# Performance work log

Measured on AMD Instinct MI355X. Metric: run time of the kernel, lower is better.

Reference implementation:

```python
import jax, jax.numpy as jnp
import numpy as np

N_NODES = 25000
N_EDGES = 400000
MUL0 = 16      # multiplicity of 0e
MUL1 = 8       # multiplicity of 1o
H = 64         # radial MLP width (= dist_embedding dim)
WEIGHT_NUMEL = MUL0*MUL0 + MUL0*MUL1 + MUL1*MUL1 + MUL1*MUL0  # 576
NUM_NEIGHBORS = 16
INV_SQRT3 = 0.57735026918962576  # w3j normalization for l=1 paths
PW0 = (1.0/24.0)**0.5  # path weight, 0e out: alpha = dim(0e)/ (16+8)
PW1 = (3.0/24.0)**0.5  # path weight, 1o out: alpha = dim(1o)/ (16+8)
SILU_NORM = 1.6791767923989418  # e3nn normalize2mom factor for silu


def _radial_mlp(d, W1, W2):
    # e3nn FullyConnectedNet([H, H, WEIGHT_NUMEL], silu): x @ W / sqrt(fan_in),
    # activation normalized to unit second moment.
    h = SILU_NORM * jax.nn.silu(d @ W1 / jnp.sqrt(jnp.asarray(H, d.dtype)))
    return h @ W2 / jnp.sqrt(jnp.asarray(H, d.dtype))


def _tensor_product(x, y, w):
    # x: [E, 40] gathered node feats; y: [E, 4] edge_attr; w: [E, 576]
    x0 = x[:, :MUL0]                        # [E,16]  0e
    x1 = x[:, MUL0:].reshape(-1, MUL1, 3)   # [E,8,3] 1o
    y0 = y[:, :1]                           # [E,1]   0e
    y1 = y[:, 1:4]                          # [E,3]   1o
    s = MUL0*MUL0
    w1 = w[:, :s].reshape(-1, MUL0, MUL0)                       # 0e*0e->0e
    w2 = w[:, s:s+MUL0*MUL1].reshape(-1, MUL0, MUL1)            # 0e*1o->1o
    s2 = s + MUL0*MUL1
    w3 = w[:, s2:s2+MUL1*MUL1].reshape(-1, MUL1, MUL1)          # 1o*0e->1o
    s3 = s2 + MUL1*MUL1
    w4 = w[:, s3:].reshape(-1, MUL1, MUL0)                      # 1o*1o->0e
    out0 = PW0 * (jnp.einsum('eu,euw->ew', x0 * y0, w1)
                  + INV_SQRT3 * jnp.einsum('eui,ei,euw->ew', x1, y1, w4))
    out1 = PW1 * INV_SQRT3 * (jnp.einsum('eu,ej,euw->ewj', x0, y1, w2)
                              + jnp.einsum('eui,euw->ewi', x1 * y0[:, :, None], w3))
    return jnp.concatenate([out0, out1.reshape(-1, MUL1*3)], axis=1)  # [E,40]


def setup_inputs() -> dict:
    key = jax.random.key(0)
    ks = jax.random.split(key, 7)
    node_input = jax.random.normal(ks[0], (N_NODES, MUL0 + 3*MUL1), jnp.float32)
    edge_src = jax.random.randint(ks[1], (N_EDGES,), 0, N_NODES)
    edge_dst = jax.random.randint(ks[2], (N_EDGES,), 0, N_NODES)
    edge_attr = jax.random.normal(ks[3], (N_EDGES, 4), jnp.float32)
    dist_embedding = jax.random.normal(ks[4], (N_EDGES, H), jnp.float32)
    W1 = jax.random.normal(ks[5], (H, H), jnp.float32)
    W2 = jax.random.normal(ks[6], (H, WEIGHT_NUMEL), jnp.float32)
    return {"node_input": node_input, "edge_src": edge_src, "edge_dst": edge_dst,
            "edge_attr": edge_attr, "dist_embedding": dist_embedding,
            "W1": W1, "W2": W2}


def reference(node_input, edge_src, edge_dst, edge_attr, dist_embedding, W1, W2):
    tp_weights = _radial_mlp(dist_embedding, W1, W2)            # [E,576]
    edge_features = _tensor_product(node_input[edge_dst], edge_attr, tp_weights)
    node_features = jax.ops.segment_sum(edge_features, edge_src,
                                        num_segments=N_NODES)
    return node_features / jnp.sqrt(jnp.asarray(NUM_NEIGHBORS, node_features.dtype))
```

## Files before the change

kernel.cpp:

```cpp
#include <hip/hip_runtime.h>

#define N_NODES 25000
#define N_EDGES 400000

static constexpr float INV_SQRT3 = 0.5773502691896257f;
static constexpr float PW0 = 0.20412414523193154f;
static constexpr float PW1 = 0.35355339059327373f;
static constexpr float SILU_NORM = 1.6791767923989418f;
static constexpr float SCC = 0.03125f;
static constexpr float KP1C = PW1 * INV_SQRT3 * SCC;
static constexpr float Q4C  = PW0 * INV_SQRT3 * SCC;

typedef __attribute__((ext_vector_type(8))) short bf16x8;
typedef __attribute__((ext_vector_type(4))) float f32x4;

__device__ __forceinline__ unsigned short f2bf(float x) {
    unsigned int u = __float_as_uint(x);
    u += 0x7FFFu + ((u >> 16) & 1u);
    return (unsigned short)(u >> 16);
}

__device__ __forceinline__ bf16x8 pack8(const float* p) {
    float4 a = *(const float4*)p, b = *(const float4*)(p + 4);
    bf16x8 r;
    r[0] = (short)f2bf(a.x); r[1] = (short)f2bf(a.y);
    r[2] = (short)f2bf(a.z); r[3] = (short)f2bf(a.w);
    r[4] = (short)f2bf(b.x); r[5] = (short)f2bf(b.y);
    r[6] = (short)f2bf(b.z); r[7] = (short)f2bf(b.w);
    return r;
}

#define WS_CNT  0
#define WS_CUR  25000
#define WS_EIDX 50000
#define WS_W1T  450000
#define WS_W2T  452048
#define WS_REQ_BYTES ((size_t)(452048 + 18432) * 4)

__global__ __launch_bounds__(256) void k_prep(const float* __restrict__ W1,
                                              const float* __restrict__ W2,
                                              unsigned short* __restrict__ W1Tg,
                                              unsigned short* __restrict__ W2Tg)
{
    const int id = blockIdx.x * 256 + threadIdx.x;
    if (id < 64 * 64) {
        const int n = id >> 6, j = id & 63;
        W1Tg[n * 64 + (j ^ ((n & 7) << 3))] = f2bf(W1[j * 64 + n]);
    }
    if (id < 576 * 64) {
        const int n = id / 64, k = id % 64;
        W2Tg[n * 64 + (k ^ ((n & 7) << 3))] = f2bf(W2[k * 576 + n]);
    }
}

__global__ __launch_bounds__(256) void k_hist(const int* __restrict__ edge_src,
                                              int* __restrict__ cnt)
{
    const int e = blockIdx.x * 256 + threadIdx.x;
    if (e < N_EDGES) atomicAdd(&cnt[edge_src[e]], 1);
}

__global__ __launch_bounds__(1024) void k_scan(const int* __restrict__ cnt,
                                               int* __restrict__ cur)
{
    __shared__ int sa[1024], sb[1024];
    const int t = threadIdx.x;
    const int base = t * 25;
    int loc[25];
    int s = 0;
#pragma unroll
    for (int q = 0; q < 25; ++q) {
        const int idx = base + q;
        const int v = (idx < N_NODES) ? cnt[idx] : 0;
        loc[q] = s; s += v;
    }
    sa[t] = s;
    __syncthreads();
    int* sp = sa; int* dp = sb;
    for (int d = 1; d < 1024; d <<= 1) {
        int v = sp[t];
        if (t >= d) v += sp[t - d];
        dp[t] = v;
        __syncthreads();
        int* tmp = sp; sp = dp; dp = tmp;
    }
    const int excl = sp[t] - s;
#pragma unroll
    for (int q = 0; q < 25; ++q) {
        const int idx = base + q;
        if (idx < N_NODES) cur[idx] = excl + loc[q];
    }
}

__global__ __launch_bounds__(256) void k_scatter(const int* __restrict__ edge_src,
                                                 int* __restrict__ cur,
                                                 int* __restrict__ eidx)
{
    const int e = blockIdx.x * 256 + threadIdx.x;
    if (e < N_EDGES) {
        const int pos = atomicAdd(&cur[edge_src[e]], 1);
        eidx[pos] = e;
    }
}

__global__ __launch_bounds__(256) void k_conv(
    const float* __restrict__ node_input,
    const int* __restrict__ edge_src,
    const int* __restrict__ edge_dst,
    const float* __restrict__ edge_attr,
    const float* __restrict__ dist_embedding,
    const unsigned short* __restrict__ W1Tg,
    const unsigned short* __restrict__ W2Tg,
    const int* __restrict__ eidx_g,
    float* __restrict__ out)
{
    __shared__ __align__(16) unsigned short sB[288 * 64];
    __shared__ __align__(16) unsigned short sH[64 * 64];
    __shared__ float xq_s[64 * 56];
    __shared__ float racc[64 * 40];
    __shared__ int   eidx_s[64], src_s[64], p0_s[64];

    const int t  = threadIdx.x;
    const int pb = blockIdx.x * 64;
    const int w = t >> 6, lane = t & 63;
    const int kgrp = lane >> 4;
    const int cl = lane & 15;

    if (t < 64) {
        const int eid = eidx_g[pb + t];
        eidx_s[t] = eid;
        src_s[t]  = edge_src[eid];
        const int dst = edge_dst[eid];
        const float4* xr = (const float4*)(node_input + (size_t)dst * 40);
        float* xd = xq_s + t * 56;
        float xx[40];
#pragma unroll
        for (int i = 0; i < 10; ++i) {
            float4 v = xr[i];
            xx[i*4+0] = v.x; xx[i*4+1] = v.y; xx[i*4+2] = v.z; xx[i*4+3] = v.w;
            *(float4*)(xd + i * 4) = v;
        }
        const float4 yv = *(const float4*)(edge_attr + (size_t)eid * 4);
        xd[48] = PW0 * SCC * yv.x;
        xd[49] = KP1C * yv.x;
        xd[50] = yv.y; xd[51] = yv.z; xd[52] = yv.w;
#pragma unroll
        for (int u = 0; u < 8; ++u)
            xd[40 + u] = yv.y * xx[16 + u*3] + yv.z * xx[16 + u*3 + 1] + yv.w * xx[16 + u*3 + 2];
    }
    {
        const uint4* s = (const uint4*)W1Tg;
        uint4* d = (uint4*)sB;
        d[t] = s[t];
        d[t + 256] = s[t + 256];
    }
    for (int i = t; i < 64 * 40; i += 256) racc[i] = 0.f;
    __syncthreads();

    {
        const int er = w * 16 + cl;
        const float* dp = dist_embedding + (size_t)eidx_s[er] * 64 + kgrp * 8;
        bf16x8 a0 = pack8(dp);
        bf16x8 a1 = pack8(dp + 32);
        const int bx = (cl & 7) << 3;
#pragma unroll
        for (int nt = 0; nt < 4; ++nt) {
            const int n = nt * 16 + cl;
            const unsigned short* bp = sB + n * 64;
            bf16x8 b0 = *(const bf16x8*)(bp + ((kgrp * 8) ^ bx));
            bf16x8 b1 = *(const bf16x8*)(bp + ((32 + kgrp * 8) ^ bx));
            f32x4 c = {0.f, 0.f, 0.f, 0.f};
            c = __builtin_amdgcn_mfma_f32_16x16x32_bf16(a0, b0, c, 0, 0, 0);
            c = __builtin_amdgcn_mfma_f32_16x16x32_bf16(a1, b1, c, 0, 0, 0);
#pragma unroll
            for (int r = 0; r < 4; ++r) {
                const float zz = 0.125f * c[r];
                const float h = SILU_NORM * __fdividef(zz, 1.f + __expf(-zz));
                const int hr = w * 16 + kgrp * 4 + r;
                const int hc = nt * 16 + cl;
                sH[hr * 64 + (hc ^ ((hr & 7) << 3))] = f2bf(h);
            }
        }
    }
    if (t < 64) {
        int p = t;
        while (p > 0 && src_s[p - 1] == src_s[t]) --p;
        p0_s[t] = p;
    }
    __syncthreads();

    const int arow = w * 16 + cl;
    const unsigned short* ap = sH + arow * 64;
    const int ax = (cl & 7) << 3;
    bf16x8 A0 = *(const bf16x8*)(ap + ((kgrp * 8) ^ ax));
    bf16x8 A1 = *(const bf16x8*)(ap + ((32 + kgrp * 8) ^ ax));

    float r1a[4] = {0,0,0,0}, r4a[4] = {0,0,0,0}, Tt[4] = {0,0,0,0};
    float P0[4] = {0,0,0,0}, P1[4] = {0,0,0,0}, P2[4] = {0,0,0,0};
    const int e0 = w * 16 + kgrp * 4;

#pragma unroll
    for (int ph = 0; ph < 2; ++ph) {
        {
            const uint4* gs = (const uint4*)(W2Tg + (size_t)ph * 18432);
            uint4* ds = (uint4*)sB;
#pragma unroll
            for (int i = 0; i < 9; ++i) ds[t + i * 256] = gs[t + i * 256];
        }
        __syncthreads();
        const int bx = (cl & 7) << 3;
#pragma unroll
        for (int nt = 0; nt < 18; ++nt) {
            const int bcol = nt * 16 + cl;
            const unsigned short* bp = sB + bcol * 64;
            bf16x8 B0 = *(const bf16x8*)(bp + ((kgrp * 8) ^ bx));
            bf16x8 B1 = *(const bf16x8*)(bp + ((32 + kgrp * 8) ^ bx));
            f32x4 c = {0.f, 0.f, 0.f, 0.f};
            c = __builtin_amdgcn_mfma_f32_16x16x32_bf16(A0, B0, c, 0, 0, 0);
            c = __builtin_amdgcn_mfma_f32_16x16x32_bf16(A1, B1, c, 0, 0, 0);
            const int gnt = ph * 18 + nt;
            if (gnt < 16) {
#pragma unroll
                for (int r = 0; r < 4; ++r) r1a[r] += xq_s[(e0 + r) * 56 + gnt] * c[r];
            } else if (gnt < 24) {
                const int u = (gnt - 16) * 2 + ((lane >> 3) & 1);
#pragma unroll
                for (int r = 0; r < 4; ++r) Tt[r] += xq_s[(e0 + r) * 56 + u] * c[r];
            } else if (gnt < 28) {
                const int u = (gnt - 24) * 2 + ((lane >> 3) & 1);
#pragma unroll
                for (int r = 0; r < 4; ++r) {
                    const float* xp = xq_s + (e0 + r) * 56 + 16 + u * 3;
                    P0[r] += xp[0] * c[r];
                    P1[r] += xp[1] * c[r];
                    P2[r] += xp[2] * c[r];
                }
            } else {
                const int u = gnt - 28;
#pragma unroll
                for (int r = 0; r < 4; ++r) r4a[r] += xq_s[(e0 + r) * 56 + 40 + u] * c[r];
            }
        }
        __syncthreads();
    }

#pragma unroll
    for (int r = 0; r < 4; ++r) {
        const int e = e0 + r;
        const float v = xq_s[e * 56 + 48] * r1a[r] + Q4C * r4a[r];
        atomicAdd(&racc[p0_s[e] * 40 + cl], v);
    }
#pragma unroll
    for (int r = 0; r < 4; ++r) {
        Tt[r] += __shfl_xor(Tt[r], 8);
        P0[r] += __shfl_xor(P0[r], 8);
        P1[r] += __shfl_xor(P1[r], 8);
        P2[r] += __shfl_xor(P2[r], 8);
    }
    if ((lane & 8) == 0) {
        const int wo = lane & 7;
#pragma unroll
        for (int r = 0; r < 4; ++r) {
            const int e = e0 + r;
            const float q3  = xq_s[e * 56 + 49];
            const float y1x = xq_s[e * 56 + 50];
            const float y1y = xq_s[e * 56 + 51];
            const float y1z = xq_s[e * 56 + 52];
            float* rp = &racc[p0_s[e] * 40 + 16 + wo * 3];
            atomicAdd(rp + 0, KP1C * y1x * Tt[r] + q3 * P0[r]);
            atomicAdd(rp + 1, KP1C * y1y * Tt[r] + q3 * P1[r]);
            atomicAdd(rp + 2, KP1C * y1z * Tt[r] + q3 * P2[r]);
        }
    }
    __syncthreads();
    if (t < 64 && p0_s[t] == t) {
        float* op = out + (size_t)src_s[t] * 40;
        const float* rp = racc + t * 40;
#pragma unroll
        for (int cc = 0; cc < 40; ++cc) atomicAdd(op + cc, rp[cc]);
    }
}

template <int NC>
__device__ __forceinline__ void gemm_cols(const float* __restrict__ base,
                                          const float (&h)[64], float (&w)[NC]) {
#pragma unroll
    for (int i = 0; i < NC; ++i) w[i] = 0.f;
#pragma unroll
    for (int k = 0; k < 64; ++k) {
        const float4* r4 = (const float4*)(base + k * 576);
        const float hk = h[k];
#pragma unroll
        for (int q = 0; q < NC / 4; ++q) {
            float4 a = r4[q];
            w[q * 4 + 0] += hk * a.x;  w[q * 4 + 1] += hk * a.y;
            w[q * 4 + 2] += hk * a.z;  w[q * 4 + 3] += hk * a.w;
        }
    }
}

__global__ __launch_bounds__(256) void conv_atomic(
    const float* __restrict__ node_input,
    const int* __restrict__ edge_src,
    const int* __restrict__ edge_dst,
    const float* __restrict__ edge_attr,
    const float* __restrict__ dist_embedding,
    const float* __restrict__ W1,
    const float* __restrict__ W2,
    float* __restrict__ out)
{
    __shared__ float sX[256 * 44];
    const int e = blockIdx.x * 256 + threadIdx.x;
    if (e >= N_EDGES) return;
    float* xs = &sX[threadIdx.x * 44];

    float z[64];
#pragma unroll
    for (int k = 0; k < 64; ++k) z[k] = 0.f;
    const float4* dp = (const float4*)(dist_embedding + (size_t)e * 64);
#pragma unroll 2
    for (int j4 = 0; j4 < 16; ++j4) {
        float4 d4 = dp[j4];
        float dj[4] = {d4.x, d4.y, d4.z, d4.w};
#pragma unroll
        for (int r = 0; r < 4; ++r) {
            const float4* w1r = (const float4*)(W1 + (j4 * 4 + r) * 64);
            const float dv = dj[r];
#pragma unroll
            for (int k4 = 0; k4 < 16; ++k4) {
                float4 a = w1r[k4];
                z[k4 * 4 + 0] += dv * a.x; z[k4 * 4 + 1] += dv * a.y;
                z[k4 * 4 + 2] += dv * a.z; z[k4 * 4 + 3] += dv * a.w;
            }
        }
    }
    float h[64];
#pragma unroll
    for (int k = 0; k < 64; ++k) {
        const float zz = 0.125f * z[k];
        h[k] = SILU_NORM * __fdividef(zz, 1.f + __expf(-zz));
    }
    const int dst = edge_dst[e];
    const float4* xr = (const float4*)(node_input + (size_t)dst * 40);
    float4* xd = (float4*)xs;
#pragma unroll
    for (int i = 0; i < 10; ++i) xd[i] = xr[i];
    const float4 yv = *(const float4*)(edge_attr + (size_t)e * 4);
    const float q0 = PW0 * yv.x * SCC;
    const float q4 = PW0 * INV_SQRT3 * SCC;
    const float q20 = KP1C * yv.y, q21 = KP1C * yv.z, q22 = KP1C * yv.w;
    const float q3 = KP1C * yv.x;
    float o0[16], o1[24];
#pragma unroll
    for (int i = 0; i < 16; ++i) o0[i] = 0.f;
#pragma unroll
    for (int i = 0; i < 24; ++i) o1[i] = 0.f;
#pragma unroll 1
    for (int u = 0; u < 16; ++u) {
        float w[16];
        gemm_cols<16>(W2 + u * 16, h, w);
        const float coef = q0 * xs[u];
#pragma unroll
        for (int i = 0; i < 16; ++i) o0[i] += coef * w[i];
    }
#pragma unroll 1
    for (int u = 0; u < 16; ++u) {
        float w[8];
        gemm_cols<8>(W2 + 256 + u * 8, h, w);
        const float xv = xs[u];
        const float c0 = q20 * xv, c1 = q21 * xv, c2 = q22 * xv;
#pragma unroll
        for (int i = 0; i < 8; ++i) {
            o1[i * 3 + 0] += c0 * w[i]; o1[i * 3 + 1] += c1 * w[i]; o1[i * 3 + 2] += c2 * w[i];
        }
    }
#pragma unroll 1
    for (int u = 0; u < 8; ++u) {
        float w[8];
        gemm_cols<8>(W2 + 384 + u * 8, h, w);
        const float c0 = q3 * xs[16 + u * 3 + 0];
        const float c1 = q3 * xs[16 + u * 3 + 1];
        const float c2 = q3 * xs[16 + u * 3 + 2];
#pragma unroll
        for (int i = 0; i < 8; ++i) {
            o1[i * 3 + 0] += c0 * w[i]; o1[i * 3 + 1] += c1 * w[i]; o1[i * 3 + 2] += c2 * w[i];
        }
    }
#pragma unroll 1
    for (int u = 0; u < 8; ++u) {
        float w[16];
        gemm_cols<16>(W2 + 448 + u * 16, h, w);
        const float b = q4 * (xs[16 + u * 3 + 0] * yv.y +
                              xs[16 + u * 3 + 1] * yv.z +
                              xs[16 + u * 3 + 2] * yv.w);
#pragma unroll
        for (int i = 0; i < 16; ++i) o0[i] += b * w[i];
    }
    const int src = edge_src[e];
    float* op = out + (size_t)src * 40;
#pragma unroll
    for (int i = 0; i < 16; ++i) atomicAdd(op + i, o0[i]);
#pragma unroll
    for (int i = 0; i < 24; ++i) atomicAdd(op + 16 + i, o1[i]);
}

extern "C" void kernel_launch(void* const* d_in, const int* in_sizes, int n_in,
                              void* d_out, int out_size, void* d_ws, size_t ws_size,
                              hipStream_t stream)
{
    const float* node_input     = (const float*)d_in[0];
    const int*   edge_src       = (const int*)d_in[1];
    const int*   edge_dst       = (const int*)d_in[2];
    const float* edge_attr      = (const float*)d_in[3];
    const float* dist_embedding = (const float*)d_in[4];
    const float* W1             = (const float*)d_in[5];
    const float* W2             = (const float*)d_in[6];
    float* out = (float*)d_out;

    hipMemsetAsync(out, 0, (size_t)out_size * sizeof(float), stream);

    if (ws_size < WS_REQ_BYTES || d_ws == nullptr) {
        dim3 grid((N_EDGES + 255) / 256);
        conv_atomic<<<grid, 256, 0, stream>>>(node_input, edge_src, edge_dst,
                                              edge_attr, dist_embedding, W1, W2, out);
        return;
    }

    int* wsI = (int*)d_ws;
    int* cnt  = wsI + WS_CNT;
    int* cur  = wsI + WS_CUR;
    int* eidx = wsI + WS_EIDX;
    unsigned short* W1Tg = (unsigned short*)(wsI + WS_W1T);
    unsigned short* W2Tg = (unsigned short*)(wsI + WS_W2T);

    hipMemsetAsync(cnt, 0, (size_t)N_NODES * sizeof(int), stream);
    k_prep<<<dim3(144), 256, 0, stream>>>(W1, W2, W1Tg, W2Tg);
    k_hist<<<dim3((N_EDGES + 255) / 256), 256, 0, stream>>>(edge_src, cnt);
    k_scan<<<dim3(1), 1024, 0, stream>>>(cnt, cur);
    k_scatter<<<dim3((N_EDGES + 255) / 256), 256, 0, stream>>>(edge_src, cur, eidx);
    k_conv<<<dim3(N_EDGES / 64), 256, 0, stream>>>(node_input, edge_src, edge_dst,
                                                   edge_attr, dist_embedding,
                                                   W1Tg, W2Tg, eidx, out);
}
```

Before: 423.6 us.

## Read MLP weights directly from global/L2 instead of staging in LDS; fuse prep with histogram

```diff
diff --git a/kernel.cpp b/kernel.cpp
--- a/kernel.cpp
+++ b/kernel.cpp
@@ -37,27 +37,23 @@
 #define WS_W2T  452048
 #define WS_REQ_BYTES ((size_t)(452048 + 18432) * 4)
 
-__global__ __launch_bounds__(256) void k_prep(const float* __restrict__ W1,
-                                              const float* __restrict__ W2,
-                                              unsigned short* __restrict__ W1Tg,
-                                              unsigned short* __restrict__ W2Tg)
+__global__ __launch_bounds__(256) void k_preph(const int* __restrict__ edge_src,
+                                               int* __restrict__ cnt,
+                                               const float* __restrict__ W1,
+                                               const float* __restrict__ W2,
+                                               unsigned short* __restrict__ W1Tg,
+                                               unsigned short* __restrict__ W2Tg)
 {
     const int id = blockIdx.x * 256 + threadIdx.x;
+    if (id < N_EDGES) atomicAdd(&cnt[edge_src[id]], 1);
     if (id < 64 * 64) {
         const int n = id >> 6, j = id & 63;
-        W1Tg[n * 64 + (j ^ ((n & 7) << 3))] = f2bf(W1[j * 64 + n]);
+        W1Tg[n * 64 + j] = f2bf(W1[j * 64 + n]);
     }
     if (id < 576 * 64) {
         const int n = id / 64, k = id % 64;
-        W2Tg[n * 64 + (k ^ ((n & 7) << 3))] = f2bf(W2[k * 576 + n]);
-    }
-}
-
-__global__ __launch_bounds__(256) void k_hist(const int* __restrict__ edge_src,
-                                              int* __restrict__ cnt)
-{
-    const int e = blockIdx.x * 256 + threadIdx.x;
-    if (e < N_EDGES) atomicAdd(&cnt[edge_src[e]], 1);
+        W2Tg[n * 64 + k] = f2bf(W2[k * 576 + n]);
+    }
 }
 
 __global__ __launch_bounds__(1024) void k_scan(const int* __restrict__ cnt,
@@ -114,7 +110,6 @@
     const int* __restrict__ eidx_g,
     float* __restrict__ out)
 {
-    __shared__ __align__(16) unsigned short sB[288 * 64];
     __shared__ __align__(16) unsigned short sH[64 * 64];
     __shared__ float xq_s[64 * 56];
     __shared__ float racc[64 * 40];
@@ -148,12 +143,6 @@
         for (int u = 0; u < 8; ++u)
             xd[40 + u] = yv.y * xx[16 + u*3] + yv.z * xx[16 + u*3 + 1] + yv.w * xx[16 + u*3 + 2];
     }
-    {
-        const uint4* s = (const uint4*)W1Tg;
-        uint4* d = (uint4*)sB;
-        d[t] = s[t];
-        d[t + 256] = s[t + 256];
-    }
     for (int i = t; i < 64 * 40; i += 256) racc[i] = 0.f;
     __syncthreads();
 
@@ -162,13 +151,11 @@
         const float* dp = dist_embedding + (size_t)eidx_s[er] * 64 + kgrp * 8;
         bf16x8 a0 = pack8(dp);
         bf16x8 a1 = pack8(dp + 32);
-        const int bx = (cl & 7) << 3;
 #pragma unroll
         for (int nt = 0; nt < 4; ++nt) {
-            const int n = nt * 16 + cl;
-            const unsigned short* bp = sB + n * 64;
-            bf16x8 b0 = *(const bf16x8*)(bp + ((kgrp * 8) ^ bx));
-            bf16x8 b1 = *(const bf16x8*)(bp + ((32 + kgrp * 8) ^ bx));
+            const unsigned short* bp = W1Tg + (nt * 16 + cl) * 64 + kgrp * 8;
+            bf16x8 b0 = *(const bf16x8*)bp;
+            bf16x8 b1 = *(const bf16x8*)(bp + 32);
             f32x4 c = {0.f, 0.f, 0.f, 0.f};
             c = __builtin_amdgcn_mfma_f32_16x16x32_bf16(a0, b0, c, 0, 0, 0);
             c = __builtin_amdgcn_mfma_f32_16x16x32_bf16(a1, b1, c, 0, 0, 0);
@@ -198,50 +185,37 @@
     float r1a[4] = {0,0,0,0}, r4a[4] = {0,0,0,0}, Tt[4] = {0,0,0,0};
     float P0[4] = {0,0,0,0}, P1[4] = {0,0,0,0}, P2[4] = {0,0,0,0};
     const int e0 = w * 16 + kgrp * 4;
-
-#pragma unroll
-    for (int ph = 0; ph < 2; ++ph) {
-        {
-            const uint4* gs = (const uint4*)(W2Tg + (size_t)ph * 18432);
-            uint4* ds = (uint4*)sB;
-#pragma unroll
-            for (int i = 0; i < 9; ++i) ds[t + i * 256] = gs[t + i * 256];
-        }
-        __syncthreads();
-        const int bx = (cl & 7) << 3;
-#pragma unroll
-        for (int nt = 0; nt < 18; ++nt) {
-            const int bcol = nt * 16 + cl;
-            const unsigned short* bp = sB + bcol * 64;
-            bf16x8 B0 = *(const bf16x8*)(bp + ((kgrp * 8) ^ bx));
-            bf16x8 B1 = *(const bf16x8*)(bp + ((32 + kgrp * 8) ^ bx));
-            f32x4 c = {0.f, 0.f, 0.f, 0.f};
-            c = __builtin_amdgcn_mfma_f32_16x16x32_bf16(A0, B0, c, 0, 0, 0);
-            c = __builtin_amdgcn_mfma_f32_16x16x32_bf16(A1, B1, c, 0, 0, 0);
-            const int gnt = ph * 18 + nt;
-            if (gnt < 16) {
-#pragma unroll
-                for (int r = 0; r < 4; ++r) r1a[r] += xq_s[(e0 + r) * 56 + gnt] * c[r];
-            } else if (gnt < 24) {
-                const int u = (gnt - 16) * 2 + ((lane >> 3) & 1);
-#pragma unroll
-                for (int r = 0; r < 4; ++r) Tt[r] += xq_s[(e0 + r) * 56 + u] * c[r];
-            } else if (gnt < 28) {
-                const int u = (gnt - 24) * 2 + ((lane >> 3) & 1);
-#pragma unroll
-                for (int r = 0; r < 4; ++r) {
-                    const float* xp = xq_s + (e0 + r) * 56 + 16 + u * 3;
-                    P0[r] += xp[0] * c[r];
-                    P1[r] += xp[1] * c[r];
-                    P2[r] += xp[2] * c[r];
-                }
-            } else {
-                const int u = gnt - 28;
-#pragma unroll
-                for (int r = 0; r < 4; ++r) r4a[r] += xq_s[(e0 + r) * 56 + 40 + u] * c[r];
+    const unsigned short* bbase = W2Tg + cl * 64 + kgrp * 8;
+
+#pragma unroll
+    for (int gnt = 0; gnt < 36; ++gnt) {
+        const unsigned short* bp = bbase + gnt * 1024;
+        bf16x8 B0 = *(const bf16x8*)bp;
+        bf16x8 B1 = *(const bf16x8*)(bp + 32);
+        f32x4 c = {0.f, 0.f, 0.f, 0.f};
+        c = __builtin_amdgcn_mfma_f32_16x16x32_bf16(A0, B0, c, 0, 0, 0);
+        c = __builtin_amdgcn_mfma_f32_16x16x32_bf16(A1, B1, c, 0, 0, 0);
+        if (gnt < 16) {
+#pragma unroll
+            for (int r = 0; r < 4; ++r) r1a[r] += xq_s[(e0 + r) * 56 + gnt] * c[r];
+        } else if (gnt < 24) {
+            const int u = (gnt - 16) * 2 + ((lane >> 3) & 1);
+#pragma unroll
+            for (int r = 0; r < 4; ++r) Tt[r] += xq_s[(e0 + r) * 56 + u] * c[r];
+        } else if (gnt < 28) {
+            const int u = (gnt - 24) * 2 + ((lane >> 3) & 1);
+#pragma unroll
+            for (int r = 0; r < 4; ++r) {
+                const float* xp = xq_s + (e0 + r) * 56 + 16 + u * 3;
+                P0[r] += xp[0] * c[r];
+                P1[r] += xp[1] * c[r];
+                P2[r] += xp[2] * c[r];
             }
-        }
-        __syncthreads();
+        } else {
+            const int u = gnt - 28;
+#pragma unroll
+            for (int r = 0; r < 4; ++r) r4a[r] += xq_s[(e0 + r) * 56 + 40 + u] * c[r];
+        }
     }
 
 #pragma unroll
@@ -434,8 +408,8 @@
     unsigned short* W2Tg = (unsigned short*)(wsI + WS_W2T);
 
     hipMemsetAsync(cnt, 0, (size_t)N_NODES * sizeof(int), stream);
-    k_prep<<<dim3(144), 256, 0, stream>>>(W1, W2, W1Tg, W2Tg);
-    k_hist<<<dim3((N_EDGES + 255) / 256), 256, 0, stream>>>(edge_src, cnt);
+    k_preph<<<dim3((N_EDGES + 255) / 256), 256, 0, stream>>>(edge_src, cnt,
+                                                             W1, W2, W1Tg, W2Tg);
     k_scan<<<dim3(1), 1024, 0, stream>>>(cnt, cur);
     k_scatter<<<dim3((N_EDGES + 255) / 256), 256, 0, stream>>>(edge_src, cur, eidx);
     k_conv<<<dim3(N_EDGES / 64), 256, 0, stream>>>(node_input, edge_src, edge_dst,
```

Measured after the change: 541.6 us. 27.9% more time.
